# Performance work log

Measured on AMD Instinct MI355X. Metric: run time of the kernel, lower is better.

Reference implementation:

```python
import jax, jax.numpy as jnp
import numpy as np

N = 524288          # query points
L = 8               # hash levels
T = 65536           # hash table size (2**16)
F = 2               # features per level
LEVELS = jnp.array([2.0, 2.6946, 3.6301, 4.8907, 6.5893, 8.8766, 11.959, 16.111], dtype=jnp.float32)
# 8 corner offsets of the unit cube
OFFSETS = jnp.array([[i, j, k] for i in (0, 1) for j in (0, 1) for k in (0, 1)], dtype=jnp.int32)  # [8,3]
PI2 = jnp.uint32(2654435761)
PI3 = jnp.uint32(805459861)


def setup_inputs() -> dict:
    key = jax.random.key(0)
    ks = jax.random.split(key, 8)
    x = jax.random.uniform(ks[0], (N, 3), dtype=jnp.float32) * 32.0
    grid = jax.random.uniform(ks[1], (L, T, F), dtype=jnp.float32) * 0.01
    d_in = L * F  # 16
    w0 = jax.random.normal(ks[2], (d_in, 64), dtype=jnp.float32) / np.sqrt(d_in)
    b0 = jnp.zeros((64,), dtype=jnp.float32)
    w1 = jax.random.normal(ks[3], (64, 32), dtype=jnp.float32) / np.sqrt(64)
    b1 = jnp.zeros((32,), dtype=jnp.float32)
    w2 = jax.random.normal(ks[4], (32, 2), dtype=jnp.float32) / np.sqrt(32)
    b2 = jnp.zeros((2,), dtype=jnp.float32)
    return {"x": x, "grid": grid, "w0": w0, "b0": b0, "w1": w1, "b1": b1, "w2": w2, "b2": b2}


def _encode(x, grid):
    # Multiresolution hash-grid lookup with trilinear interpolation.
    xs = x[:, None, :] * LEVELS[None, :, None]                  # [N,L,3]
    x0 = jnp.floor(xs).astype(jnp.int32)                        # [N,L,3]
    f = xs - x0                                                 # fractional part
    corners = x0[:, :, None, :] + OFFSETS[None, None, :, :]     # [N,L,8,3]
    c = corners.astype(jnp.uint32)
    # NGP spatial hash (Eq. 4): (x + y*pi2 + z*pi3) mod T, uint32 wraparound
    idx = (c[..., 0] + c[..., 1] * PI2 + c[..., 2] * PI3) % jnp.uint32(T)  # [N,L,8]
    feats = grid[jnp.arange(L)[None, :, None], idx]             # [N,L,8,F]
    # trilinear weights: prod over xyz of (f if corner bit set else 1-f)
    fb = f[:, :, None, :]
    w = jnp.prod(jnp.where(OFFSETS[None, None].astype(bool), fb, 1.0 - fb), axis=-1)  # [N,L,8]
    enc = jnp.einsum('nlc,nlcf->nlf', w, feats)                 # [N,L,F]
    return enc.reshape(x.shape[0], L * F)                       # [N,16]


def reference(x, grid, w0, b0, w1, b1, w2, b2):
    enc = _encode(x, grid)
    h = jax.nn.leaky_relu(enc @ w0 + b0)
    h = jax.nn.leaky_relu(h @ w1 + b1)
    out = h @ w2 + b2                                           # [N,2]
    sigma, alpha = out[:, 0], out[:, 1]
    sigma_clip, alpha_scale = -1.0, 0.1
    return (jnp.where(sigma > sigma_clip, sigma, 0.0),
            jnp.minimum(0.0, alpha) * alpha_scale,
            jnp.zeros_like(sigma))
```

## Files before the change

### kernel.cpp

```cpp
#include <hip/hip_runtime.h>
#include <hip/hip_fp16.h>


#define NPTS 524288
#define TTAB 65536
#define PI2 2654435761u
#define PI3 805459861u

typedef float vf2 __attribute__((ext_vector_type(2)));
typedef float vf4 __attribute__((ext_vector_type(4)));

__device__ __forceinline__ vf4 load16_a8(const float* p) {
    vf4 r; __builtin_memcpy(&r, p, 16); return r;
}
__device__ __forceinline__ uint2 load8_a4(const void* p) {
    uint2 r; __builtin_memcpy(&r, p, 8); return r;
}

__global__ __launch_bounds__(256) void convert_grid(
    const float* __restrict__ g, __half* __restrict__ h)
{
    const int i = blockIdx.x * 256 + threadIdx.x;
    const float4 v = ((const float4*)g)[i];
    union { __half2 h2[2]; uint2 u; } cv;
    cv.h2[0] = __floats2half2_rn(v.x, v.y);
    cv.h2[1] = __floats2half2_rn(v.z, v.w);
    ((uint2*)h)[i] = cv.u;
}

template <bool F16>
__global__ __launch_bounds__(256) void ngp_kernel(
    const float* __restrict__ x,
    const float* __restrict__ gridp,
    const float* __restrict__ w0,
    const float* __restrict__ b0,
    const float* __restrict__ w1,
    const float* __restrict__ b1,
    const float* __restrict__ w2,
    const float* __restrict__ b2,
    float* __restrict__ out,
    const __half* __restrict__ htab)
{
    const int n = blockIdx.x * 256 + threadIdx.x;
    const float px = __builtin_nontemporal_load(&x[n * 3 + 0]);
    const float py = __builtin_nontemporal_load(&x[n * 3 + 1]);
    const float pz = __builtin_nontemporal_load(&x[n * 3 + 2]);

    const float levels[8] = {2.0f, 2.6946f, 3.6301f, 4.8907f,
                             6.5893f, 8.8766f, 11.959f, 16.111f};

    float fxs[8], fys[8], fzs[8];
    unsigned hb[8];
    #pragma unroll
    for (int l = 0; l < 8; ++l) {
        const float lev = levels[l];
        float xs0 = px * lev, xs1 = py * lev, xs2 = pz * lev;
        float fl0 = floorf(xs0), fl1 = floorf(xs1), fl2 = floorf(xs2);
        fxs[l] = xs0 - fl0;
        fys[l] = xs1 - fl1;
        fzs[l] = xs2 - fl2;
        unsigned cx = (unsigned)(int)fl0;
        unsigned cy = (unsigned)(int)fl1;
        unsigned cz = (unsigned)(int)fl2;
        hb[l] = cx + cy * PI2 + cz * PI3;
    }

    vf2 enc2[8];

    if constexpr (F16) {
        uint2 praw[32];
        #pragma unroll
        for (int l = 0; l < 8; ++l) {
            #pragma unroll
            for (int p = 0; p < 4; ++p) {
                const unsigned delta = ((p >> 1) ? PI2 : 0u)
                                     + ((p & 1) ? PI3 : 0u);
                unsigned b = (hb[l] + delta) & (TTAB - 1u);
                unsigned lidx = b - ((b == (TTAB - 1u)) ? 1u : 0u);
                praw[l * 4 + p] = load8_a4((const unsigned char*)htab
                                  + (((unsigned)(l * TTAB) + lidx) << 2));
            }
        }

        __builtin_amdgcn_sched_barrier(0);

        #pragma unroll
        for (int l = 0; l < 8; ++l) {
            const float fx = fxs[l], fy = fys[l], fz = fzs[l];
            const float gx = 1.f - fx, gy = 1.f - fy, gz = 1.f - fz;
            const vf2 first = {gridp[l * TTAB * 2 + 0],
                               gridp[l * TTAB * 2 + 1]};
            vf2 e = {0.f, 0.f};
            #pragma unroll
            for (int p = 0; p < 4; ++p) {
                const unsigned delta = ((p >> 1) ? PI2 : 0u)
                                     + ((p & 1) ? PI3 : 0u);
                unsigned b = (hb[l] + delta) & (TTAB - 1u);
                const bool wrap = (b == (TTAB - 1u));
                uint2 pr = praw[l * 4 + p];
                union { unsigned u; __half2 h; } ul, uh;
                ul.u = pr.x; uh.u = pr.y;
                vf2 lo = {__low2float(ul.h), __high2float(ul.h)};
                vf2 hi = {__low2float(uh.h), __high2float(uh.h)};
                vf2 c0 = wrap ? hi : lo;
                vf2 c1 = wrap ? first : hi;
                const float wyz = ((p >> 1) ? fy : gy) * ((p & 1) ? fz : gz);
                const float wl = gx * wyz, wr = fx * wyz;
                e = __builtin_elementwise_fma((vf2){wl, wl}, c0, e);
                e = __builtin_elementwise_fma((vf2){wr, wr}, c1, e);
            }
            enc2[l] = e;
        }
    } else {
        #pragma unroll
        for (int l = 0; l < 8; ++l) {
            const float fx = fxs[l], fy = fys[l], fz = fzs[l];
            const float gx = 1.f - fx, gy = 1.f - fy, gz = 1.f - fz;
            const vf2 first = {gridp[l * TTAB * 2 + 0],
                               gridp[l * TTAB * 2 + 1]};
            vf2 e = {0.f, 0.f};
            #pragma unroll
            for (int p = 0; p < 4; ++p) {
                const unsigned delta = ((p >> 1) ? PI2 : 0u)
                                     + ((p & 1) ? PI3 : 0u);
                unsigned b = (hb[l] + delta) & (TTAB - 1u);
                const bool wrap = (b == (TTAB - 1u));
                unsigned lidx = b - (wrap ? 1u : 0u);
                vf4 pr = load16_a8(gridp + ((unsigned)(l * TTAB) + lidx) * 2u);
                vf2 lo = {pr.x, pr.y}, hi = {pr.z, pr.w};
                vf2 c0 = wrap ? hi : lo;
                vf2 c1 = wrap ? first : hi;
                const float wyz = ((p >> 1) ? fy : gy) * ((p & 1) ? fz : gz);
                const float wl = gx * wyz, wr = fx * wyz;
                e = __builtin_elementwise_fma((vf2){wl, wl}, c0, e);
                e = __builtin_elementwise_fma((vf2){wr, wr}, c1, e);
            }
            enc2[l] = e;
        }
    }

    float enc[16];
    #pragma unroll
    for (int l = 0; l < 8; ++l) { enc[2 * l] = enc2[l].x; enc[2 * l + 1] = enc2[l].y; }

    float h1[32];
    #pragma unroll
    for (int k = 0; k < 32; ++k) h1[k] = 0.f;

    #pragma unroll 2
    for (int j = 0; j < 64; ++j) {
        float a = b0[j];
        #pragma unroll
        for (int k = 0; k < 16; ++k)
            a = fmaf(w0[k * 64 + j], enc[k], a);
        a = fmaf(0.01f, fminf(a, 0.f), fmaxf(a, 0.f));

        #pragma unroll
        for (int k = 0; k < 32; ++k)
            h1[k] = fmaf(w1[j * 32 + k], a, h1[k]);
    }

    float s0 = b2[0], s1 = b2[1];
    #pragma unroll
    for (int k = 0; k < 32; ++k) {
        float hk = h1[k] + b1[k];
        hk = fmaf(0.01f, fminf(hk, 0.f), fmaxf(hk, 0.f));
        s0 = fmaf(hk, w2[k * 2 + 0], s0);
        s1 = fmaf(hk, w2[k * 2 + 1], s1);
    }

    __builtin_nontemporal_store((s0 > -1.0f) ? s0 : 0.0f, &out[n]);
    __builtin_nontemporal_store(fminf(0.0f, s1) * 0.1f, &out[NPTS + n]);
    __builtin_nontemporal_store(0.0f, &out[2 * NPTS + n]);
}

extern "C" void kernel_launch(void* const* d_in, const int* in_sizes, int n_in,
                              void* d_out, int out_size, void* d_ws, size_t ws_size,
                              hipStream_t stream) {
    const float* x    = (const float*)d_in[0];
    const float* grid = (const float*)d_in[1];
    const float* w0   = (const float*)d_in[2];
    const float* b0   = (const float*)d_in[3];
    const float* w1   = (const float*)d_in[4];
    const float* b1   = (const float*)d_in[5];
    const float* w2   = (const float*)d_in[6];
    const float* b2   = (const float*)d_in[7];
    float* out = (float*)d_out;

    const size_t tab_bytes = (size_t)8 * TTAB * 2 * sizeof(__half);
    if (ws_size >= tab_bytes) {
        __half* htab = (__half*)d_ws;
        convert_grid<<<1024, 256, 0, stream>>>(grid, htab);
        ngp_kernel<true><<<NPTS / 256, 256, 0, stream>>>(
            x, grid, w0, b0, w1, b1, w2, b2, out, htab);
    } else {
        ngp_kernel<false><<<NPTS / 256, 256, 0, stream>>>(
            x, grid, w0, b0, w1, b1, w2, b2, out, nullptr);
    }
}
```

Measured before the change: 151.0 us.

## Build per-level fp16 supertable so each level needs two 16-byte gathers

A preprocessing kernel builds, for every hash bucket, a 16-byte record holding the fp16 features of the four corners that differ in x and y (offsets 0, 1, PI2, PI2+1 mod T). Each level's trilinear lookup then takes two gathers (base and base+PI3) instead of four 8-byte loads, and the wrap special case goes away. The record table is 8 MB instead of the 2 MB fp16 table, and building it adds work on every call. The MLP is also rewritten with packed two-wide FMAs and a transposed w0 so weight loads are vectorized.

```diff
diff --git a/kernel.cpp b/kernel.cpp
--- a/kernel.cpp
+++ b/kernel.cpp
@@ -6,6 +6,7 @@
 #define TTAB 65536
 #define PI2 2654435761u
 #define PI3 805459861u
+#define MASK16 65535u
 
 typedef float vf2 __attribute__((ext_vector_type(2)));
 typedef float vf4 __attribute__((ext_vector_type(4)));
@@ -13,33 +14,59 @@
 __device__ __forceinline__ vf4 load16_a8(const float* p) {
     vf4 r; __builtin_memcpy(&r, p, 16); return r;
 }
-__device__ __forceinline__ uint2 load8_a4(const void* p) {
-    uint2 r; __builtin_memcpy(&r, p, 8); return r;
-}
-
-__global__ __launch_bounds__(256) void convert_grid(
-    const float* __restrict__ g, __half* __restrict__ h)
+__device__ __forceinline__ unsigned f2h2(float a, float b) {
+    __half2 h = __floats2half2_rn(a, b);
+    unsigned u; __builtin_memcpy(&u, &h, 4); return u;
+}
+__device__ __forceinline__ vf2 h2f2(unsigned u) {
+    __half2 h; __builtin_memcpy(&h, &u, 4);
+    float2 f = __half22float2(h);
+    return (vf2){f.x, f.y};
+}
+
+__global__ __launch_bounds__(256) void build_supertable(
+    const float* __restrict__ g, uint4* __restrict__ V)
+{
+    const unsigned i = blockIdx.x * 256 + threadIdx.x;
+    const unsigned b = i & MASK16;
+    const unsigned C2 = PI2 & MASK16;
+    const float2* __restrict__ gl = (const float2*)g + (i - b);
+    float2 e00 = gl[b];
+    float2 e10 = gl[(b + 1u) & MASK16];
+    float2 e01 = gl[(b + C2) & MASK16];
+    float2 e11 = gl[(b + C2 + 1u) & MASK16];
+    uint4 o;
+    o.x = f2h2(e00.x, e00.y);
+    o.y = f2h2(e10.x, e10.y);
+    o.z = f2h2(e01.x, e01.y);
+    o.w = f2h2(e11.x, e11.y);
+    V[i] = o;
+}
+
+__global__ __launch_bounds__(256) void pack_w0t(
+    const float* __restrict__ w0, float* __restrict__ w0t)
 {
     const int i = blockIdx.x * 256 + threadIdx.x;
-    const float4 v = ((const float4*)g)[i];
-    union { __half2 h2[2]; uint2 u; } cv;
-    cv.h2[0] = __floats2half2_rn(v.x, v.y);
-    cv.h2[1] = __floats2half2_rn(v.z, v.w);
-    ((uint2*)h)[i] = cv.u;
-}
-
-template <bool F16>
+    if (i < 512) {
+        const int j = i >> 3, m = i & 7;
+        w0t[i * 2 + 0] = w0[(2 * m) * 64 + j];
+        w0t[i * 2 + 1] = w0[(2 * m + 1) * 64 + j];
+    }
+}
+
+template <bool SUPER>
 __global__ __launch_bounds__(256) void ngp_kernel(
     const float* __restrict__ x,
     const float* __restrict__ gridp,
     const float* __restrict__ w0,
-    const float* __restrict__ b0,
+    const float* __restrict__ b0p,
     const float* __restrict__ w1,
     const float* __restrict__ b1,
     const float* __restrict__ w2,
     const float* __restrict__ b2,
     float* __restrict__ out,
-    const __half* __restrict__ htab)
+    const uint4* __restrict__ V,
+    const float* __restrict__ w0t)
 {
     const int n = blockIdx.x * 256 + threadIdx.x;
     const float px = __builtin_nontemporal_load(&x[n * 3 + 0]);
@@ -67,23 +94,39 @@
 
     vf2 enc2[8];
 
-    if constexpr (F16) {
-        uint2 praw[32];
+    if constexpr (SUPER) {
+        const unsigned C3 = PI3 & MASK16;
+        uint4 praw[16];
         #pragma unroll
         for (int l = 0; l < 8; ++l) {
+            unsigned bb0 = hb[l] & MASK16;
+            unsigned bb1 = (bb0 + C3) & MASK16;
+            praw[2 * l + 0] = V[l * TTAB + (int)bb0];
+            praw[2 * l + 1] = V[l * TTAB + (int)bb1];
+        }
+        __builtin_amdgcn_sched_barrier(0);
+
+        #pragma unroll
+        for (int l = 0; l < 8; ++l) {
+            const float fx = fxs[l], fy = fys[l], fz = fzs[l];
+            const float gx = 1.f - fx, gy = 1.f - fy, gz = 1.f - fz;
+            const float w00 = gx * gy, w10 = fx * gy;
+            const float w01 = gx * fy, w11 = fx * fy;
+            vf2 e = {0.f, 0.f};
             #pragma unroll
-            for (int p = 0; p < 4; ++p) {
-                const unsigned delta = ((p >> 1) ? PI2 : 0u)
-                                     + ((p & 1) ? PI3 : 0u);
-                unsigned b = (hb[l] + delta) & (TTAB - 1u);
-                unsigned lidx = b - ((b == (TTAB - 1u)) ? 1u : 0u);
-                praw[l * 4 + p] = load8_a4((const unsigned char*)htab
-                                  + (((unsigned)(l * TTAB) + lidx) << 2));
+            for (int k = 0; k < 2; ++k) {
+                const uint4 q = praw[2 * l + k];
+                vf2 t = {0.f, 0.f};
+                t = __builtin_elementwise_fma((vf2){w00, w00}, h2f2(q.x), t);
+                t = __builtin_elementwise_fma((vf2){w10, w10}, h2f2(q.y), t);
+                t = __builtin_elementwise_fma((vf2){w01, w01}, h2f2(q.z), t);
+                t = __builtin_elementwise_fma((vf2){w11, w11}, h2f2(q.w), t);
+                const float kf = k ? fz : gz;
+                e = __builtin_elementwise_fma((vf2){kf, kf}, t, e);
             }
-        }
-
-        __builtin_amdgcn_sched_barrier(0);
-
+            enc2[l] = e;
+        }
+    } else {
         #pragma unroll
         for (int l = 0; l < 8; ++l) {
             const float fx = fxs[l], fy = fys[l], fz = fzs[l];
@@ -95,36 +138,8 @@
             for (int p = 0; p < 4; ++p) {
                 const unsigned delta = ((p >> 1) ? PI2 : 0u)
                                      + ((p & 1) ? PI3 : 0u);
-                unsigned b = (hb[l] + delta) & (TTAB - 1u);
-                const bool wrap = (b == (TTAB - 1u));
-                uint2 pr = praw[l * 4 + p];
-                union { unsigned u; __half2 h; } ul, uh;
-                ul.u = pr.x; uh.u = pr.y;
-                vf2 lo = {__low2float(ul.h), __high2float(ul.h)};
-                vf2 hi = {__low2float(uh.h), __high2float(uh.h)};
-                vf2 c0 = wrap ? hi : lo;
-                vf2 c1 = wrap ? first : hi;
-                const float wyz = ((p >> 1) ? fy : gy) * ((p & 1) ? fz : gz);
-                const float wl = gx * wyz, wr = fx * wyz;
-                e = __builtin_elementwise_fma((vf2){wl, wl}, c0, e);
-                e = __builtin_elementwise_fma((vf2){wr, wr}, c1, e);
-            }
-            enc2[l] = e;
-        }
-    } else {
-        #pragma unroll
-        for (int l = 0; l < 8; ++l) {
-            const float fx = fxs[l], fy = fys[l], fz = fzs[l];
-            const float gx = 1.f - fx, gy = 1.f - fy, gz = 1.f - fz;
-            const vf2 first = {gridp[l * TTAB * 2 + 0],
-                               gridp[l * TTAB * 2 + 1]};
-            vf2 e = {0.f, 0.f};
-            #pragma unroll
-            for (int p = 0; p < 4; ++p) {
-                const unsigned delta = ((p >> 1) ? PI2 : 0u)
-                                     + ((p & 1) ? PI3 : 0u);
-                unsigned b = (hb[l] + delta) & (TTAB - 1u);
-                const bool wrap = (b == (TTAB - 1u));
+                unsigned b = (hb[l] + delta) & MASK16;
+                const bool wrap = (b == MASK16);
                 unsigned lidx = b - (wrap ? 1u : 0u);
                 vf4 pr = load16_a8(gridp + ((unsigned)(l * TTAB) + lidx) * 2u);
                 vf2 lo = {pr.x, pr.y}, hi = {pr.z, pr.w};
@@ -139,34 +154,48 @@
         }
     }
 
-    float enc[16];
+    vf2 h1p[16];
     #pragma unroll
-    for (int l = 0; l < 8; ++l) { enc[2 * l] = enc2[l].x; enc[2 * l + 1] = enc2[l].y; }
-
-    float h1[32];
-    #pragma unroll
-    for (int k = 0; k < 32; ++k) h1[k] = 0.f;
+    for (int m = 0; m < 16; ++m) h1p[m] = (vf2){0.f, 0.f};
 
     #pragma unroll 2
     for (int j = 0; j < 64; ++j) {
-        float a = b0[j];
-        #pragma unroll
-        for (int k = 0; k < 16; ++k)
-            a = fmaf(w0[k * 64 + j], enc[k], a);
+        vf2 acc = {b0p[j], 0.f};
+        if constexpr (true) {}
+        const vf2* __restrict__ wj =
+            SUPER ? (const vf2*)&w0t[j * 16] : nullptr;
+        #pragma unroll
+        for (int m = 0; m < 8; ++m) {
+            vf2 wv;
+            if constexpr (SUPER) {
+                wv = wj[m];
+            } else {
+                wv = (vf2){w0[(2 * m) * 64 + j], w0[(2 * m + 1) * 64 + j]};
+            }
+            acc = __builtin_elementwise_fma(enc2[m], wv, acc);
+        }
+        float a = acc.x + acc.y;
         a = fmaf(0.01f, fminf(a, 0.f), fmaxf(a, 0.f));
 
-        #pragma unroll
-        for (int k = 0; k < 32; ++k)
-            h1[k] = fmaf(w1[j * 32 + k], a, h1[k]);
-    }
-
+        vf2 av = {a, a};
+        const vf2* __restrict__ w1j = (const vf2*)&w1[j * 32];
+        #pragma unroll
+        for (int m = 0; m < 16; ++m)
+            h1p[m] = __builtin_elementwise_fma(av, w1j[m], h1p[m]);
+    }
+
+    const vf2* __restrict__ b1p = (const vf2*)b1;
     float s0 = b2[0], s1 = b2[1];
     #pragma unroll
-    for (int k = 0; k < 32; ++k) {
-        float hk = h1[k] + b1[k];
-        hk = fmaf(0.01f, fminf(hk, 0.f), fmaxf(hk, 0.f));
-        s0 = fmaf(hk, w2[k * 2 + 0], s0);
-        s1 = fmaf(hk, w2[k * 2 + 1], s1);
+    for (int m = 0; m < 16; ++m) {
+        vf2 hk = h1p[m] + b1p[m];
+        vf2 pos = __builtin_elementwise_max(hk, (vf2){0.f, 0.f});
+        vf2 neg = __builtin_elementwise_min(hk, (vf2){0.f, 0.f});
+        hk = __builtin_elementwise_fma((vf2){0.01f, 0.01f}, neg, pos);
+        s0 = fmaf(hk.x, w2[(2 * m) * 2 + 0], s0);
+        s1 = fmaf(hk.x, w2[(2 * m) * 2 + 1], s1);
+        s0 = fmaf(hk.y, w2[(2 * m + 1) * 2 + 0], s0);
+        s1 = fmaf(hk.y, w2[(2 * m + 1) * 2 + 1], s1);
     }
 
     __builtin_nontemporal_store((s0 > -1.0f) ? s0 : 0.0f, &out[n]);
@@ -187,14 +216,17 @@
     const float* b2   = (const float*)d_in[7];
     float* out = (float*)d_out;
 
-    const size_t tab_bytes = (size_t)8 * TTAB * 2 * sizeof(__half);
-    if (ws_size >= tab_bytes) {
-        __half* htab = (__half*)d_ws;
-        convert_grid<<<1024, 256, 0, stream>>>(grid, htab);
+    const size_t vt_bytes  = (size_t)8 * TTAB * 16;
+    const size_t w0t_bytes = 512 * 2 * sizeof(float);
+    if (ws_size >= vt_bytes + w0t_bytes) {
+        uint4* V   = (uint4*)d_ws;
+        float* w0t = (float*)((char*)d_ws + vt_bytes);
+        build_supertable<<<2048, 256, 0, stream>>>(grid, V);
+        pack_w0t<<<2, 256, 0, stream>>>(w0, w0t);
         ngp_kernel<true><<<NPTS / 256, 256, 0, stream>>>(
-            x, grid, w0, b0, w1, b1, w2, b2, out, htab);
+            x, grid, w0, b0, w1, b1, w2, b2, out, V, w0t);
     } else {
         ngp_kernel<false><<<NPTS / 256, 256, 0, stream>>>(
-            x, grid, w0, b0, w1, b1, w2, b2, out, nullptr);
-    }
-}
+            x, grid, w0, b0, w1, b1, w2, b2, out, nullptr, nullptr);
+    }
+}
```

Result: slower. 154.8 us (+2.5%).
